# Performance work log

Hardware: AMD Instinct MI355X
Metric: run time of the kernel (lower is better)

## Reference

```python
import jax, jax.numpy as jnp
import numpy as np

B, C, N, D, K, M, E, G = 2, 64, 16384, 3, 128, 1, 262144, 3


def setup_inputs() -> dict:
    key = jax.random.key(0)
    ks = jax.random.split(key, 15)
    scale = 1.0 / (C * C)
    return {
        "x": jax.random.normal(ks[0], (B, C, N), jnp.float32),
        "nodes": jax.random.uniform(ks[1], (B, N, D), jnp.float32),
        "node_weights": jax.random.uniform(ks[2], (B, N, M), jnp.float32),
        "geo": jax.random.normal(ks[3], (B, G, N), jnp.float32),
        "directed_edges": jax.random.randint(ks[4], (B, E, 2), 0, N, jnp.int32),
        "edge_gradient_weights": 0.1 * jax.random.normal(ks[5], (B, E, D), jnp.float32),
        "modes": jax.random.normal(ks[6], (K, D, M), jnp.float32),
        "weights_c": scale * jax.random.uniform(ks[7], (C, C, K, M), jnp.float32),
        "weights_s": scale * jax.random.uniform(ks[8], (C, C, K, M), jnp.float32),
        "weights_0": scale * jax.random.uniform(ks[9], (C, C, 1, M), jnp.float32),
        "W": jax.random.normal(ks[10], (C, C), jnp.float32) / np.sqrt(C),
        "gw": jax.random.normal(ks[11], (C, C * D), jnp.float32) / np.sqrt(C * D),
        "geo_wx": jax.random.normal(ks[12], (C, G), jnp.float32) / np.sqrt(G),
        "wx": jax.random.normal(ks[13], (C, C), jnp.float32) / np.sqrt(C),
        "w2": jax.random.normal(ks[14], (C, C), jnp.float32) / np.sqrt(C),
    }


def reference(x, nodes, node_weights, geo, directed_edges, edge_gradient_weights,
              modes, weights_c, weights_s, weights_0, W, gw, geo_wx, wx, w2):
    # ---- Fourier bases: cos(kx), sin(kx), 1 -------------------------------
    temp = jnp.einsum('bxd,kdw->bxkw', nodes, modes)          # [B,N,K,M]
    bases_c, bases_s = jnp.cos(temp), jnp.sin(temp)
    b, n = temp.shape[0], temp.shape[1]
    bases_0 = jnp.ones((b, n, 1, temp.shape[3]), temp.dtype)
    nw = node_weights[:, :, None, :]                          # quadrature weights
    wb_c, wb_s, wb_0 = bases_c * nw, bases_s * nw, bases_0 * nw

    # ---- Spectral convolution (non-uniform Fourier neural layer) ----------
    x_c = jnp.einsum('bix,bxkw->bikw', x, wb_c)
    x_s = -jnp.einsum('bix,bxkw->bikw', x, wb_s)
    x_0 = jnp.einsum('bix,bxkw->bikw', x, wb_0)
    f_c = jnp.einsum('bikw,iokw->bokw', x_c, weights_c) - jnp.einsum('bikw,iokw->bokw', x_s, weights_s)
    f_s = jnp.einsum('bikw,iokw->bokw', x_s, weights_c) + jnp.einsum('bikw,iokw->bokw', x_c, weights_s)
    f_0 = jnp.einsum('bikw,iokw->bokw', x_0, weights_0)
    x1 = (jnp.einsum('bokw,bxkw->box', f_0, bases_0)
          + 2.0 * jnp.einsum('bokw,bxkw->box', f_c, bases_c)
          - 2.0 * jnp.einsum('bokw,bxkw->box', f_s, bases_s))

    # ---- Pointwise linear W ----------------------------------------------
    x2 = jnp.einsum('oi,bix->box', W, x)

    # ---- Least-squares gradient via edge gather + scatter-add -------------
    fT = jnp.transpose(x, (0, 2, 1))                          # [B,N,C]
    tgt, src = directed_edges[..., 0], directed_edges[..., 1]  # [B,E]
    f_src = jnp.take_along_axis(fT, src[:, :, None], axis=1)   # [B,E,C]
    f_tgt = jnp.take_along_axis(fT, tgt[:, :, None], axis=1)
    df = f_src - f_tgt
    # message[b,e,c,d] = w[b,e,d] * df[b,e,c], flattened c-major -> [B,E,C*D]
    msg = (df[..., :, None] * edge_gradient_weights[..., None, :]).reshape(b, tgt.shape[1], -1)
    gradf = jnp.zeros((b, n, msg.shape[-1]), msg.dtype).at[jnp.arange(b)[:, None], tgt].add(msg)
    x3 = jnp.einsum('og,bng->bon', gw, gradf)                  # [B,C,N]

    # ---- Geo embedding: w2 @ (softsign(geo_wx@geo) * (wx@x)) --------------
    h = jax.nn.soft_sign(jnp.einsum('og,bgx->box', geo_wx, geo)) * jnp.einsum('oi,bix->box', wx, x)
    x4 = jnp.einsum('oi,bix->box', w2, h)

    return jax.nn.gelu(x1 + x2 + x3 + x4, approximate=False)
```

## Files before the change

### kernel.cpp

```cpp
#include <hip/hip_runtime.h>
#include <hip/hip_fp16.h>
#include <math.h>

#define BB 2
#define CC 64
#define NN 16384
#define DD 3
#define KK 128
#define EE 262144
#define GG 3
#define PP 128
#define LL (NN/PP)
#define KTOT 576

typedef short bf16x8 __attribute__((ext_vector_type(8)));
typedef float f32x4  __attribute__((ext_vector_type(4)));

__device__ __forceinline__ short f2bf(float f) {
    unsigned u = __float_as_uint(f);
    u += 0x7FFF + ((u >> 16) & 1);
    return (short)(u >> 16);
}

constexpr size_t OFF_XT   = 0;
constexpr size_t OFF_PC   = OFF_XT   + (size_t)BB*NN*CC;
constexpr size_t OFF_PS   = OFF_PC   + (size_t)BB*PP*CC*KK;
constexpr size_t OFF_BIN4 = OFF_PC;
constexpr size_t OFF_AC   = OFF_PS   + (size_t)BB*PP*CC*KK;
constexpr size_t OFF_AS   = OFF_AC   + (size_t)BB*CC*KK;
constexpr size_t OFF_F0   = OFF_AS   + (size_t)BB*CC*KK;
constexpr size_t OFF_X0   = OFF_F0   + (size_t)BB*CC;
constexpr size_t OFF_CNT  = OFF_X0   + (size_t)BB*CC;
constexpr size_t OFF_OFFS = OFF_CNT  + (size_t)BB*NN;
constexpr size_t OFF_RANK = OFF_OFFS + (size_t)BB*NN;
constexpr size_t OFF_GRT  = OFF_RANK + (size_t)BB*EE;
constexpr size_t OFF_APAN = OFF_GRT  + (size_t)BB*192*NN;
constexpr size_t OFF_GWXT = OFF_APAN + (size_t)BB*KTOT*CC;

__global__ void k_prep(const float* __restrict__ W, const float* __restrict__ gw,
                       const float* __restrict__ geo_wx, const float* __restrict__ w2,
                       float* gwxT, short* ApanB) {
    int idx = blockIdx.x*256 + threadIdx.x;
    if (idx < CC*CC) {
        int j = idx>>6, o = idx&63;
        short wv  = f2bf(W[o*CC+j]);
        short w2v = f2bf(w2[o*CC+j]);
        ApanB[((size_t)(0*CC+o))*KTOT + 256 + j] = wv;
        ApanB[((size_t)(1*CC+o))*KTOT + 256 + j] = wv;
        ApanB[((size_t)(0*CC+o))*KTOT + 320 + j] = w2v;
        ApanB[((size_t)(1*CC+o))*KTOT + 320 + j] = w2v;
    }
    if (idx < CC*CC*DD) {
        int g = idx>>6, o = idx&63;
        short gv = f2bf(gw[o*(CC*DD)+g]);
        ApanB[((size_t)(0*CC+o))*KTOT + 384 + g] = gv;
        ApanB[((size_t)(1*CC+o))*KTOT + 384 + g] = gv;
    }
    if (idx < GG*CC) { int g = idx>>6, i = idx&63; gwxT[idx] = geo_wx[i*GG+g]; }
}

__global__ void __launch_bounds__(256) k_pre(const float* __restrict__ x,
                                             const float* __restrict__ nwt,
                                             const int* __restrict__ edges,
                                             float* __restrict__ xT,
                                             float* __restrict__ x0,
                                             int* __restrict__ counts,
                                             int* __restrict__ rank) {
    int blk = blockIdx.x;
    int tid = threadIdx.x;
    __shared__ float tile[64][65];
    __shared__ float red[256];
    if (blk < BB*(NN/64)) {
        int b = blk / (NN/64);
        int n0 = (blk % (NN/64)) * 64;
        int c = tid & 63, r4 = tid >> 6;
        for (int rr = 0; rr < 16; rr++) {
            int i = r4*16 + rr;
            tile[i][c] = x[((size_t)b*CC + i)*NN + n0 + c];
        }
        __syncthreads();
        for (int rr = 0; rr < 16; rr++) {
            int nn = r4*16 + rr;
            xT[((size_t)b*NN + n0 + nn)*CC + c] = tile[c][nn];
        }
    } else if (blk < BB*(NN/64) + BB*CC) {
        int bi = blk - BB*(NN/64);
        int b = bi >> 6, i = bi & 63;
        const float4* __restrict__ xr = (const float4*)&x[((size_t)b*CC + i)*NN];
        const float4* __restrict__ wr = (const float4*)&nwt[(size_t)b*NN];
        float s = 0.f;
        for (int t = tid; t < NN/4; t += 256) {
            float4 xv = xr[t];
            float4 wv = wr[t];
            s += xv.x*wv.x + xv.y*wv.y + xv.z*wv.z + xv.w*wv.w;
        }
        red[tid] = s;
        __syncthreads();
        for (int off = 128; off > 0; off >>= 1) {
            if (tid < off) red[tid] += red[tid+off];
            __syncthreads();
        }
        if (tid == 0) x0[b*CC + i] = red[0];
    } else {
        int idx = (blk - (BB*(NN/64) + BB*CC))*256 + tid;
        if (idx < BB*EE) {
            int tgt = edges[(size_t)idx*2 + 0];
            int b = idx / EE;
            rank[idx] = atomicAdd(&counts[b*NN + tgt], 1);
        }
    }
}

__global__ void __launch_bounds__(256) k_a(const float* __restrict__ xT,
                                           const float* __restrict__ nodes,
                                           const float* __restrict__ nwt,
                                           const float* __restrict__ modes,
                                           float* __restrict__ pc, float* __restrict__ ps) {
    int bc = blockIdx.x;
    int b = bc / PP, chunk = bc % PP;
    int k0 = blockIdx.y * 64;
    int nbase = chunk * LL;
    int tid = threadIdx.x;
    int lane = tid & 63;
    int w = tid >> 6;
    int col = lane & 15;
    int quad = lane >> 4;

    __shared__ __align__(16) short Axw[64*136];
    __shared__ __align__(16) short Bc [64*136];
    __shared__ __align__(16) short Bsn[64*136];
    __shared__ float ndl[LL*3];

    for (int e = tid; e < LL*3; e += 256) ndl[e] = nodes[((size_t)b*NN + nbase)*3 + e];
#pragma unroll
    for (int s = 0; s < 32; s++) {
        int e = tid + s*256;
        int n = e >> 6, i = e & 63;
        float v = xT[((size_t)b*NN + nbase + n)*CC + i] * nwt[b*NN + nbase + n];
        Axw[i*136 + n] = f2bf(v);
    }
    __syncthreads();
#pragma unroll
    for (int s = 0; s < 32; s++) {
        int e = tid + s*256;
        int n = e & 127, kl = e >> 7;
        int k = k0 + kl;
        float t = ndl[n*3+0]*modes[k*3+0] + ndl[n*3+1]*modes[k*3+1]
                + ndl[n*3+2]*modes[k*3+2];
        Bc [kl*136 + n] = f2bf(__cosf(t));
        Bsn[kl*136 + n] = f2bf(__sinf(t));
    }
    __syncthreads();

    f32x4 ac[4], as4[4];
#pragma unroll
    for (int it = 0; it < 4; it++)
#pragma unroll
        for (int r = 0; r < 4; r++) { ac[it][r] = 0.f; as4[it][r] = 0.f; }

    int rowB = (w*16 + col)*136;
#pragma unroll
    for (int ns = 0; ns < 4; ns++) {
        int koff = ns*32 + quad*8;
        bf16x8 bcf = *(bf16x8*)&Bc [rowB + koff];
        bf16x8 bsf = *(bf16x8*)&Bsn[rowB + koff];
#pragma unroll
        for (int it = 0; it < 4; it++) {
            bf16x8 af = *(bf16x8*)&Axw[(it*16 + col)*136 + koff];
            ac[it]  = __builtin_amdgcn_mfma_f32_16x16x32_bf16(af, bcf, ac[it], 0, 0, 0);
            as4[it] = __builtin_amdgcn_mfma_f32_16x16x32_bf16(af, bsf, as4[it], 0, 0, 0);
        }
    }
    int base = (b*PP + chunk)*CC;
    int kw = k0 + w*16 + col;
#pragma unroll
    for (int it = 0; it < 4; it++) {
#pragma unroll
        for (int r = 0; r < 4; r++) {
            int i = it*16 + quad*4 + r;
            pc[(size_t)(base + i)*KK + kw] = ac[it][r];
            ps[(size_t)(base + i)*KK + kw] = as4[it][r];
        }
    }
}

__global__ void k_ared(const float* __restrict__ pc, const float* __restrict__ ps,
                       float* __restrict__ Ac, float* __restrict__ As) {
    int idx = blockIdx.x*256 + threadIdx.x;
    if (idx >= BB*CC*KK) return;
    int b = idx / (CC*KK);
    int r = idx % (CC*KK);
    float sc = 0.f, ss = 0.f;
    for (int ch = 0; ch < PP; ch++) {
        size_t o = ((size_t)(b*PP + ch)*CC)*KK + r;
        sc += pc[o]; ss += ps[o];
    }
    Ac[idx] = sc; As[idx] = ss;
}

__global__ void __launch_bounds__(256) k_b(const float* __restrict__ Ac, const float* __restrict__ As_,
                                           const float* __restrict__ wc, const float* __restrict__ wsw,
                                           const float* __restrict__ w0, const float* __restrict__ x0,
                                           short* __restrict__ ApanB, float* __restrict__ f0) {
    int idx = blockIdx.x;
    int b = idx / (CC*2);
    int rem = idx % (CC*2);
    int o = rem >> 1, khalf = rem & 1;
    int tid = threadIdx.x;
    int kl = tid & 63, ig = tid >> 6;
    int k = khalf*64 + kl;
    float fc = 0.f, fs = 0.f;
    for (int ii = 0; ii < 16; ii++) {
        int i = ig*16 + ii;
        float a_c = Ac[(b*CC+i)*KK + k];
        float a_s = As_[(b*CC+i)*KK + k];
        float wcc = wc[((size_t)(i*CC+o))*KK + k];
        float wss = wsw[((size_t)(i*CC+o))*KK + k];
        fc += a_c*wcc + a_s*wss;
        fs += a_c*wss - a_s*wcc;
    }
    __shared__ float rc[256], rs[256];
    __shared__ float f0s[64];
    rc[tid] = fc; rs[tid] = fs;
    if (khalf == 0 && tid < 64) f0s[tid] = x0[b*CC + tid] * w0[tid*CC + o];
    __syncthreads();
    if (ig == 0) {
        fc = rc[kl] + rc[64+kl] + rc[128+kl] + rc[192+kl];
        fs = rs[kl] + rs[64+kl] + rs[128+kl] + rs[192+kl];
        unsigned pk = (unsigned)(unsigned short)f2bf(2.f*fc)
                    | ((unsigned)(unsigned short)f2bf(-2.f*fs) << 16);
        ((unsigned*)ApanB)[((size_t)(b*CC + o))*(KTOT/2) + k] = pk;
    }
    if (khalf == 0 && tid == 0) {
        float acc = 0.f;
        for (int i = 0; i < 64; i++) acc += f0s[i];
        f0[b*CC+o] = acc;
    }
}

__global__ void __launch_bounds__(1024) k_scan(const int* __restrict__ counts,
                                               int* __restrict__ offsets) {
    __shared__ int part[1024];
    int b = blockIdx.x;
    int tid = threadIdx.x;
    int base = tid*16;
    int loc[16]; int s = 0;
    for (int j = 0; j < 16; j++) { loc[j] = counts[b*NN + base + j]; s += loc[j]; }
    part[tid] = s;
    __syncthreads();
    for (int off = 1; off < 1024; off <<= 1) {
        int v = (tid >= off) ? part[tid-off] : 0;
        __syncthreads();
        part[tid] += v;
        __syncthreads();
    }
    int excl = part[tid] - s;
    for (int j = 0; j < 16; j++) {
        offsets[b*NN+base+j] = excl;
        excl += loc[j];
    }
}

__global__ void k_fill(const int* __restrict__ edges, const float* __restrict__ egw,
                       const int* __restrict__ offs, const int* __restrict__ rank,
                       float4* __restrict__ bin4) {
    int idx = blockIdx.x*256 + threadIdx.x;
    if (idx >= BB*EE) return;
    int b = idx / EE;
    int tgt = edges[(size_t)idx*2+0];
    int src = edges[(size_t)idx*2+1];
    const float* __restrict__ ew = &egw[(size_t)idx*3];
    float w0 = ew[0], w1 = ew[1], w2 = ew[2];
    int pos = offs[b*NN+tgt] + rank[idx];
    bin4[(size_t)b*EE + pos] = make_float4(__int_as_float(src), w0, w1, w2);
}

#define ECAP 1024
__global__ void __launch_bounds__(256) k_edge(const float* __restrict__ xT,
                                              const int* __restrict__ offsets,
                                              const float4* __restrict__ bin4,
                                              float* __restrict__ gradfT) {
    int blk = blockIdx.x;
    int b = blk / (NN/16);
    int n0 = (blk % (NN/16)) * 16;
    int tid = threadIdx.x;
    int lane = tid & 63;
    int w = tid >> 6;
    __shared__ float4 ebuf[ECAP];
    __shared__ float gl[16][193];
    __shared__ int soff[17];
    if (tid < 16) soff[tid] = offsets[b*NN + n0 + tid];
    if (tid == 16) soff[16] = (n0 + 16 < NN) ? offsets[b*NN + n0 + 16] : EE;
    __syncthreads();
    int base = soff[0];
    int end  = soff[16];
    const float* __restrict__ xTb = &xT[(size_t)b*NN*CC + lane];

    float a0[4], a1[4], a2[4], s0[4], s1[4], s2[4];
#pragma unroll
    for (int q = 0; q < 4; q++) { a0[q]=a1[q]=a2[q]=0.f; s0[q]=s1[q]=s2[q]=0.f; }

    for (int cs = base; cs < end; cs += ECAP) {
        int ce = min(cs + ECAP, end);
        __syncthreads();
        for (int t = cs + tid; t < ce; t += 256)
            ebuf[t - cs] = bin4[(size_t)b*EE + t];
        __syncthreads();
#pragma unroll
        for (int q = 0; q < 4; q++) {
            int nl = w*4 + q;
            int js = max(soff[nl], cs);
            int je = min(soff[nl+1], ce);
#pragma unroll 4
            for (int j = js; j < je; j++) {
                float4 e = ebuf[j - cs];
                int src = __float_as_int(e.x);
                float xs = xTb[(size_t)src*CC];
                a0[q] = fmaf(xs, e.y, a0[q]);
                a1[q] = fmaf(xs, e.z, a1[q]);
                a2[q] = fmaf(xs, e.w, a2[q]);
                s0[q] += e.y; s1[q] += e.z; s2[q] += e.w;
            }
        }
    }
    __syncthreads();
#pragma unroll
    for (int q = 0; q < 4; q++) {
        int nl = w*4 + q;
        float xtgt = xTb[(size_t)(n0 + nl)*CC];
        gl[nl][lane*3+0] = a0[q] - xtgt*s0[q];
        gl[nl][lane*3+1] = a1[q] - xtgt*s1[q];
        gl[nl][lane*3+2] = a2[q] - xtgt*s2[q];
    }
    __syncthreads();
    for (int t = tid; t < 16*192; t += 256) {
        int g = t >> 4, nl = t & 15;
        gradfT[((size_t)b*192+g)*NN + n0 + nl] = gl[nl][g];
    }
}

#define KCB 64
__global__ void __launch_bounds__(256) k_gemm(const float* __restrict__ x,
                                              const float* __restrict__ nodes,
                                              const float* __restrict__ modes,
                                              const float* __restrict__ geo,
                                              const float* __restrict__ gradfT,
                                              const short* __restrict__ ApanB,
                                              const float* __restrict__ f0,
                                              const float* __restrict__ wx,
                                              const float* __restrict__ gwxT,
                                              float* __restrict__ out) {
    int blk = blockIdx.x;
    int b  = blk >> 8;
    int n0 = (blk & 255) * 64;
    int tid = threadIdx.x;
    int lane = tid & 63;
    int w = tid >> 6;
    int w16 = w * 16;
    int col  = lane & 15;
    int quad = lane >> 4;
    int quad8 = quad * 8;
    int quad4 = quad * 4;

    __shared__ __align__(16) short As[64*72];
    __shared__ __align__(16) short Bs[64*72];
    __shared__ __align__(16) short Ws[64*72];
    __shared__ float ndl[192];
    __shared__ float geo3[192];

    for (int e = tid; e < 4096; e += 256) {
        int i = e >> 6, j = e & 63;
        Ws[i*72 + j] = f2bf(wx[i*64 + j]);
    }
    if (tid < 192) ndl[tid]  = nodes[((size_t)b*NN + n0)*3 + tid];
    if (tid < 192) geo3[tid] = geo[((size_t)b*GG + (tid >> 6))*NN + n0 + (tid & 63)];

    f32x4 acc[4], xwa[4];
    float f0v[4];
#pragma unroll
    for (int r = 0; r < 4; r++) f0v[r] = f0[b*CC + w16 + quad4 + r];
#pragma unroll
    for (int nt = 0; nt < 4; nt++) {
#pragma unroll
        for (int r = 0; r < 4; r++) { acc[nt][r] = f0v[r]; xwa[nt][r] = 0.f; }
    }

    const short* __restrict__ Ab = ApanB + ((size_t)b*CC)*KTOT;

    for (int c = 0; c < 9; c++) {
        __syncthreads();
        for (int e = tid; e < 512; e += 256) {
            int o = e >> 3, seg = e & 7;
            *(uint4*)&As[o*72 + seg*8] =
                *(const uint4*)&Ab[(size_t)o*KTOT + c*64 + seg*8];
        }
        if (c < 4) {
#pragma unroll
            for (int s = 0; s < 8; s++) {
                int e = tid + s*256;
                int n = e >> 5, kpl = e & 31;
                int kp = c*32 + kpl;
                float t = ndl[n*3+0]*modes[kp*3+0] + ndl[n*3+1]*modes[kp*3+1]
                        + ndl[n*3+2]*modes[kp*3+2];
                unsigned pk = (unsigned)(unsigned short)f2bf(__cosf(t))
                            | ((unsigned)(unsigned short)f2bf(__sinf(t)) << 16);
                ((unsigned*)Bs)[n*36 + kpl] = pk;
            }
        } else if (c == 5) {
#pragma unroll
            for (int r = 0; r < 4; r++) {
                int i = w16 + quad4 + r;
                float g0 = gwxT[i], g1 = gwxT[64+i], g2 = gwxT[128+i];
#pragma unroll
                for (int nt = 0; nt < 4; nt++) {
                    int n = nt*16 + col;
                    float t = g0*geo3[n] + g1*geo3[64+n] + g2*geo3[128+n];
                    float ssv = t / (1.f + fabsf(t));
                    Bs[n*72 + i] = f2bf(ssv * xwa[nt][r]);
                }
            }
        } else {
            const float* __restrict__ src = (c == 4)
                ? &x[(size_t)b*CC*NN]
                : &gradfT[((size_t)b*192 + (c-6)*64)*NN];
#pragma unroll
            for (int s = 0; s < 16; s++) {
                int e = tid + s*256;
                int r = e >> 6, n = e & 63;
                Bs[n*72 + r] = f2bf(src[(size_t)r*NN + n0 + n]);
            }
        }
        __syncthreads();
        int rowA = (w16 + col) * 72;
#pragma unroll
        for (int ko = 0; ko < 2; ko++) {
            int koff = ko*32 + quad8;
            bf16x8 af = *(bf16x8*)&As[rowA + koff];
            if (c == 4) {
                bf16x8 wf = *(bf16x8*)&Ws[rowA + koff];
#pragma unroll
                for (int nt = 0; nt < 4; nt++) {
                    bf16x8 bfv = *(bf16x8*)&Bs[(nt*16 + col)*72 + koff];
                    acc[nt] = __builtin_amdgcn_mfma_f32_16x16x32_bf16(af, bfv, acc[nt], 0, 0, 0);
                    xwa[nt] = __builtin_amdgcn_mfma_f32_16x16x32_bf16(wf, bfv, xwa[nt], 0, 0, 0);
                }
            } else {
#pragma unroll
                for (int nt = 0; nt < 4; nt++) {
                    bf16x8 bfv = *(bf16x8*)&Bs[(nt*16 + col)*72 + koff];
                    acc[nt] = __builtin_amdgcn_mfma_f32_16x16x32_bf16(af, bfv, acc[nt], 0, 0, 0);
                }
            }
        }
    }
#pragma unroll
    for (int nt = 0; nt < 4; nt++) {
#pragma unroll
        for (int r = 0; r < 4; r++) {
            int o = w16 + quad4 + r;
            float v = acc[nt][r];
            float g = 0.5f * v * (1.f + erff(v * 0.70710678118654752f));
            out[((size_t)b*CC + o)*NN + n0 + nt*16 + col] = g;
        }
    }
}

extern "C" void kernel_launch(void* const* d_in, const int* in_sizes, int n_in,
                              void* d_out, int out_size, void* d_ws, size_t ws_size,
                              hipStream_t stream) {
    const float* x      = (const float*)d_in[0];
    const float* nodes  = (const float*)d_in[1];
    const float* nwt    = (const float*)d_in[2];
    const float* geo    = (const float*)d_in[3];
    const int*   edges  = (const int*)d_in[4];
    const float* egw    = (const float*)d_in[5];
    const float* modes  = (const float*)d_in[6];
    const float* wc     = (const float*)d_in[7];
    const float* wsw    = (const float*)d_in[8];
    const float* w0     = (const float*)d_in[9];
    const float* W      = (const float*)d_in[10];
    const float* gw     = (const float*)d_in[11];
    const float* geo_wx = (const float*)d_in[12];
    const float* wx     = (const float*)d_in[13];
    const float* w2     = (const float*)d_in[14];

    float* ws   = (float*)d_ws;
    float* xT   = ws + OFF_XT;
    float* pc   = ws + OFF_PC;
    float* ps   = ws + OFF_PS;
    float* Ac   = ws + OFF_AC;
    float* As_  = ws + OFF_AS;
    float* f0   = ws + OFF_F0;
    float* x0   = ws + OFF_X0;
    int*  counts = (int*)(ws + OFF_CNT);
    int*  offs   = (int*)(ws + OFF_OFFS);
    int*  rank   = (int*)(ws + OFF_RANK);
    float4* bin4 = (float4*)(ws + OFF_BIN4);
    float* gradfT = ws + OFF_GRT;
    short* ApanB  = (short*)(ws + OFF_APAN);
    float* gwxT   = ws + OFF_GWXT;
    float* out  = (float*)d_out;

    hipMemsetAsync(counts, 0, (size_t)(BB*NN)*sizeof(int), stream);

    k_prep <<<48, 256, 0, stream>>>(W, gw, geo_wx, w2, gwxT, ApanB);
    k_pre  <<<BB*(NN/64) + BB*CC + (BB*EE)/256, 256, 0, stream>>>(x, nwt, edges, xT, x0,
                                                                  counts, rank);
    k_a    <<<dim3(BB*PP, 2), 256, 0, stream>>>(xT, nodes, nwt, modes, pc, ps);
    k_ared <<<(BB*CC*KK)/256, 256, 0, stream>>>(pc, ps, Ac, As_);
    k_b    <<<BB*CC*2, 256, 0, stream>>>(Ac, As_, wc, wsw, w0, x0, ApanB, f0);
    k_scan <<<BB, 1024, 0, stream>>>(counts, offs);
    k_fill <<<(BB*EE)/256, 256, 0, stream>>>(edges, egw, offs, rank, bin4);
    k_edge <<<BB*(NN/16), 256, 0, stream>>>(xT, offs, bin4, gradfT);
    k_gemm <<<BB*(NN/64), 256, 0, stream>>>(x, nodes, modes, geo, gradfT, ApanB, f0,
                                            wx, gwxT, out);
}
```

Before: 221.7 us.

## Store intermediates as bf16 in node-major layout and fold prep into k_pre

The transposed x, the node-weighted x, and the gradient buffer are now written as bf16, with gradf stored node-major. This lets k_a, k_edge and k_gemm stage tiles with 16-byte vector loads instead of strided fp32 scalar loads and per-element conversion. The weight-prep kernel is merged into k_pre as extra blocks, removing one launch. Intermediate traffic roughly halves, but the edge gather now reads bf16-rounded x, which may shift gradient accuracy slightly.

```diff
diff --git a/kernel.cpp b/kernel.cpp
--- a/kernel.cpp
+++ b/kernel.cpp
@@ -21,9 +21,13 @@
     u += 0x7FFF + ((u >> 16) & 1);
     return (short)(u >> 16);
 }
-
-constexpr size_t OFF_XT   = 0;
-constexpr size_t OFF_PC   = OFF_XT   + (size_t)BB*NN*CC;
+__device__ __forceinline__ float bf2f(unsigned short u) {
+    return __uint_as_float(((unsigned)u) << 16);
+}
+
+constexpr size_t OFF_XB   = 0;
+constexpr size_t OFF_XWB  = OFF_XB   + (size_t)BB*NN*32;
+constexpr size_t OFF_PC   = OFF_XWB  + (size_t)BB*NN*32;
 constexpr size_t OFF_PS   = OFF_PC   + (size_t)BB*PP*CC*KK;
 constexpr size_t OFF_BIN4 = OFF_PC;
 constexpr size_t OFF_AC   = OFF_PS   + (size_t)BB*PP*CC*KK;
@@ -33,39 +37,24 @@
 constexpr size_t OFF_CNT  = OFF_X0   + (size_t)BB*CC;
 constexpr size_t OFF_OFFS = OFF_CNT  + (size_t)BB*NN;
 constexpr size_t OFF_RANK = OFF_OFFS + (size_t)BB*NN;
-constexpr size_t OFF_GRT  = OFF_RANK + (size_t)BB*EE;
-constexpr size_t OFF_APAN = OFF_GRT  + (size_t)BB*192*NN;
-constexpr size_t OFF_GWXT = OFF_APAN + (size_t)BB*KTOT*CC;
-
-__global__ void k_prep(const float* __restrict__ W, const float* __restrict__ gw,
-                       const float* __restrict__ geo_wx, const float* __restrict__ w2,
-                       float* gwxT, short* ApanB) {
-    int idx = blockIdx.x*256 + threadIdx.x;
-    if (idx < CC*CC) {
-        int j = idx>>6, o = idx&63;
-        short wv  = f2bf(W[o*CC+j]);
-        short w2v = f2bf(w2[o*CC+j]);
-        ApanB[((size_t)(0*CC+o))*KTOT + 256 + j] = wv;
-        ApanB[((size_t)(1*CC+o))*KTOT + 256 + j] = wv;
-        ApanB[((size_t)(0*CC+o))*KTOT + 320 + j] = w2v;
-        ApanB[((size_t)(1*CC+o))*KTOT + 320 + j] = w2v;
-    }
-    if (idx < CC*CC*DD) {
-        int g = idx>>6, o = idx&63;
-        short gv = f2bf(gw[o*(CC*DD)+g]);
-        ApanB[((size_t)(0*CC+o))*KTOT + 384 + g] = gv;
-        ApanB[((size_t)(1*CC+o))*KTOT + 384 + g] = gv;
-    }
-    if (idx < GG*CC) { int g = idx>>6, i = idx&63; gwxT[idx] = geo_wx[i*GG+g]; }
-}
+constexpr size_t OFF_GRB  = OFF_RANK + (size_t)BB*EE;
+constexpr size_t OFF_APAN = OFF_GRB  + (size_t)BB*NN*96;
+constexpr size_t OFF_GWXT = OFF_APAN + (size_t)BB*KTOT*CC/2;
 
 __global__ void __launch_bounds__(256) k_pre(const float* __restrict__ x,
                                              const float* __restrict__ nwt,
                                              const int* __restrict__ edges,
-                                             float* __restrict__ xT,
+                                             const float* __restrict__ W,
+                                             const float* __restrict__ gw,
+                                             const float* __restrict__ geo_wx,
+                                             const float* __restrict__ w2,
+                                             unsigned short* __restrict__ xB,
+                                             unsigned short* __restrict__ xwB,
                                              float* __restrict__ x0,
                                              int* __restrict__ counts,
-                                             int* __restrict__ rank) {
+                                             int* __restrict__ rank,
+                                             float* __restrict__ gwxT,
+                                             short* __restrict__ ApanB) {
     int blk = blockIdx.x;
     int tid = threadIdx.x;
     __shared__ float tile[64][65];
@@ -78,10 +67,15 @@
             int i = r4*16 + rr;
             tile[i][c] = x[((size_t)b*CC + i)*NN + n0 + c];
         }
+        float nwv = nwt[b*NN + n0 + c];
         __syncthreads();
         for (int rr = 0; rr < 16; rr++) {
             int nn = r4*16 + rr;
-            xT[((size_t)b*NN + n0 + nn)*CC + c] = tile[c][nn];
+            xB[((size_t)b*NN + n0 + nn)*64 + c] = (unsigned short)f2bf(tile[c][nn]);
+        }
+        for (int rr = 0; rr < 16; rr++) {
+            int i = r4*16 + rr;
+            xwB[((size_t)b*CC + i)*NN + n0 + c] = (unsigned short)f2bf(tile[i][c] * nwv);
         }
     } else if (blk < BB*(NN/64) + BB*CC) {
         int bi = blk - BB*(NN/64);
@@ -101,19 +95,36 @@
             __syncthreads();
         }
         if (tid == 0) x0[b*CC + i] = red[0];
-    } else {
+    } else if (blk < BB*(NN/64) + BB*CC + (BB*EE)/256) {
         int idx = (blk - (BB*(NN/64) + BB*CC))*256 + tid;
         if (idx < BB*EE) {
             int tgt = edges[(size_t)idx*2 + 0];
             int b = idx / EE;
             rank[idx] = atomicAdd(&counts[b*NN + tgt], 1);
         }
-    }
-}
-
-__global__ void __launch_bounds__(256) k_a(const float* __restrict__ xT,
+    } else {
+        int idx = (blk - (BB*(NN/64) + BB*CC + (BB*EE)/256))*256 + tid;
+        if (idx < CC*CC) {
+            int j = idx>>6, o = idx&63;
+            short wv  = f2bf(W[o*CC+j]);
+            short w2v = f2bf(w2[o*CC+j]);
+            ApanB[((size_t)(0*CC+o))*KTOT + 256 + j] = wv;
+            ApanB[((size_t)(1*CC+o))*KTOT + 256 + j] = wv;
+            ApanB[((size_t)(0*CC+o))*KTOT + 320 + j] = w2v;
+            ApanB[((size_t)(1*CC+o))*KTOT + 320 + j] = w2v;
+        }
+        if (idx < CC*CC*DD) {
+            int g = idx>>6, o = idx&63;
+            short gv = f2bf(gw[o*(CC*DD)+g]);
+            ApanB[((size_t)(0*CC+o))*KTOT + 384 + g] = gv;
+            ApanB[((size_t)(1*CC+o))*KTOT + 384 + g] = gv;
+        }
+        if (idx < GG*CC) { int g = idx>>6, i = idx&63; gwxT[idx] = geo_wx[i*GG+g]; }
+    }
+}
+
+__global__ void __launch_bounds__(256) k_a(const unsigned short* __restrict__ xwB,
                                            const float* __restrict__ nodes,
-                                           const float* __restrict__ nwt,
                                            const float* __restrict__ modes,
                                            float* __restrict__ pc, float* __restrict__ ps) {
     int bc = blockIdx.x;
@@ -133,11 +144,11 @@
 
     for (int e = tid; e < LL*3; e += 256) ndl[e] = nodes[((size_t)b*NN + nbase)*3 + e];
 #pragma unroll
-    for (int s = 0; s < 32; s++) {
+    for (int s = 0; s < 4; s++) {
         int e = tid + s*256;
-        int n = e >> 6, i = e & 63;
-        float v = xT[((size_t)b*NN + nbase + n)*CC + i] * nwt[b*NN + nbase + n];
-        Axw[i*136 + n] = f2bf(v);
+        int i = e >> 4, seg = e & 15;
+        *(uint4*)&Axw[i*136 + seg*8] =
+            *(const uint4*)&xwB[((size_t)b*CC + i)*NN + nbase + seg*8];
     }
     __syncthreads();
 #pragma unroll
@@ -276,10 +287,10 @@
 }
 
 #define ECAP 1024
-__global__ void __launch_bounds__(256) k_edge(const float* __restrict__ xT,
+__global__ void __launch_bounds__(256) k_edge(const unsigned short* __restrict__ xB,
                                               const int* __restrict__ offsets,
                                               const float4* __restrict__ bin4,
-                                              float* __restrict__ gradfT) {
+                                              unsigned short* __restrict__ gradfB) {
     int blk = blockIdx.x;
     int b = blk / (NN/16);
     int n0 = (blk % (NN/16)) * 16;
@@ -294,7 +305,7 @@
     __syncthreads();
     int base = soff[0];
     int end  = soff[16];
-    const float* __restrict__ xTb = &xT[(size_t)b*NN*CC + lane];
+    const unsigned short* __restrict__ xBb = xB + (size_t)b*NN*64 + lane;
 
     float a0[4], a1[4], a2[4], s0[4], s1[4], s2[4];
 #pragma unroll
@@ -315,7 +326,7 @@
             for (int j = js; j < je; j++) {
                 float4 e = ebuf[j - cs];
                 int src = __float_as_int(e.x);
-                float xs = xTb[(size_t)src*CC];
+                float xs = bf2f(xBb[(size_t)src*64]);
                 a0[q] = fmaf(xs, e.y, a0[q]);
                 a1[q] = fmaf(xs, e.z, a1[q]);
                 a2[q] = fmaf(xs, e.w, a2[q]);
@@ -327,24 +338,23 @@
 #pragma unroll
     for (int q = 0; q < 4; q++) {
         int nl = w*4 + q;
-        float xtgt = xTb[(size_t)(n0 + nl)*CC];
+        float xtgt = bf2f(xBb[(size_t)(n0 + nl)*64]);
         gl[nl][lane*3+0] = a0[q] - xtgt*s0[q];
         gl[nl][lane*3+1] = a1[q] - xtgt*s1[q];
         gl[nl][lane*3+2] = a2[q] - xtgt*s2[q];
     }
     __syncthreads();
     for (int t = tid; t < 16*192; t += 256) {
-        int g = t >> 4, nl = t & 15;
-        gradfT[((size_t)b*192+g)*NN + n0 + nl] = gl[nl][g];
-    }
-}
-
-#define KCB 64
-__global__ void __launch_bounds__(256) k_gemm(const float* __restrict__ x,
+        int nl = t / 192, g = t % 192;
+        gradfB[((size_t)(b*NN + n0 + nl))*192 + g] = (unsigned short)f2bf(gl[nl][g]);
+    }
+}
+
+__global__ void __launch_bounds__(256) k_gemm(const unsigned short* __restrict__ xB,
                                               const float* __restrict__ nodes,
                                               const float* __restrict__ modes,
                                               const float* __restrict__ geo,
-                                              const float* __restrict__ gradfT,
+                                              const unsigned short* __restrict__ gradfB,
                                               const short* __restrict__ ApanB,
                                               const float* __restrict__ f0,
                                               const float* __restrict__ wx,
@@ -406,6 +416,12 @@
                             | ((unsigned)(unsigned short)f2bf(__sinf(t)) << 16);
                 ((unsigned*)Bs)[n*36 + kpl] = pk;
             }
+        } else if (c == 4) {
+            for (int e = tid; e < 512; e += 256) {
+                int n = e >> 3, seg = e & 7;
+                *(uint4*)&Bs[n*72 + seg*8] =
+                    *(const uint4*)&xB[((size_t)(b*NN + n0 + n))*64 + seg*8];
+            }
         } else if (c == 5) {
 #pragma unroll
             for (int r = 0; r < 4; r++) {
@@ -420,14 +436,11 @@
                 }
             }
         } else {
-            const float* __restrict__ src = (c == 4)
-                ? &x[(size_t)b*CC*NN]
-                : &gradfT[((size_t)b*192 + (c-6)*64)*NN];
-#pragma unroll
-            for (int s = 0; s < 16; s++) {
-                int e = tid + s*256;
-                int r = e >> 6, n = e & 63;
-                Bs[n*72 + r] = f2bf(src[(size_t)r*NN + n0 + n]);
+            const unsigned short* __restrict__ src = gradfB + (size_t)(c-6)*64;
+            for (int e = tid; e < 512; e += 256) {
+                int n = e >> 3, seg = e & 7;
+                *(uint4*)&Bs[n*72 + seg*8] =
+                    *(const uint4*)&src[((size_t)(b*NN + n0 + n))*192 + seg*8];
             }
         }
         __syncthreads();
@@ -485,7 +498,8 @@
     const float* w2     = (const float*)d_in[14];
 
     float* ws   = (float*)d_ws;
-    float* xT   = ws + OFF_XT;
+    unsigned short* xB  = (unsigned short*)(ws + OFF_XB);
+    unsigned short* xwB = (unsigned short*)(ws + OFF_XWB);
     float* pc   = ws + OFF_PC;
     float* ps   = ws + OFF_PS;
     float* Ac   = ws + OFF_AC;
@@ -496,22 +510,22 @@
     int*  offs   = (int*)(ws + OFF_OFFS);
     int*  rank   = (int*)(ws + OFF_RANK);
     float4* bin4 = (float4*)(ws + OFF_BIN4);
-    float* gradfT = ws + OFF_GRT;
+    unsigned short* gradfB = (unsigned short*)(ws + OFF_GRB);
     short* ApanB  = (short*)(ws + OFF_APAN);
     float* gwxT   = ws + OFF_GWXT;
     float* out  = (float*)d_out;
 
     hipMemsetAsync(counts, 0, (size_t)(BB*NN)*sizeof(int), stream);
 
-    k_prep <<<48, 256, 0, stream>>>(W, gw, geo_wx, w2, gwxT, ApanB);
-    k_pre  <<<BB*(NN/64) + BB*CC + (BB*EE)/256, 256, 0, stream>>>(x, nwt, edges, xT, x0,
-                                                                  counts, rank);
-    k_a    <<<dim3(BB*PP, 2), 256, 0, stream>>>(xT, nodes, nwt, modes, pc, ps);
+    int npre = BB*(NN/64) + BB*CC + (BB*EE)/256 + 48;
+    k_pre  <<<npre, 256, 0, stream>>>(x, nwt, edges, W, gw, geo_wx, w2,
+                                      xB, xwB, x0, counts, rank, gwxT, ApanB);
+    k_a    <<<dim3(BB*PP, 2), 256, 0, stream>>>(xwB, nodes, modes, pc, ps);
     k_ared <<<(BB*CC*KK)/256, 256, 0, stream>>>(pc, ps, Ac, As_);
     k_b    <<<BB*CC*2, 256, 0, stream>>>(Ac, As_, wc, wsw, w0, x0, ApanB, f0);
     k_scan <<<BB, 1024, 0, stream>>>(counts, offs);
     k_fill <<<(BB*EE)/256, 256, 0, stream>>>(edges, egw, offs, rank, bin4);
-    k_edge <<<BB*(NN/16), 256, 0, stream>>>(xT, offs, bin4, gradfT);
-    k_gemm <<<BB*(NN/64), 256, 0, stream>>>(x, nodes, modes, geo, gradfT, ApanB, f0,
+    k_edge <<<BB*(NN/16), 256, 0, stream>>>(xB, offs, bin4, gradfB);
+    k_gemm <<<BB*(NN/64), 256, 0, stream>>>(xB, nodes, modes, geo, gradfB, ApanB, f0,
                                             wx, gwxT, out);
 }
```

After: 216.6 us. 2.3% less time.
